# Performance work log

Measured on AMD Instinct MI355X. Metric: run time of the kernel, lower is better.

The kernel has to match this reference:

```python
import jax, jax.numpy as jnp
import numpy as np

D_MODEL = 1024
NUM_HEADS = 16
D_K = D_MODEL // NUM_HEADS


def setup_inputs() -> dict:
    key = jax.random.key(0)
    ks = jax.random.split(key, 11)
    B, S, D = 2, 2048, D_MODEL
    scale = 1.0 / np.sqrt(D)
    inp = {
        'q': jax.random.normal(ks[0], (B, S, D), jnp.float32),
        'k': jax.random.normal(ks[1], (B, S, D), jnp.float32),
        'v': jax.random.normal(ks[2], (B, S, D), jnp.float32),
        'wq': jax.random.normal(ks[3], (D, D), jnp.float32) * scale,
        'bq': jnp.zeros((D,), jnp.float32),
        'wk': jax.random.normal(ks[4], (D, D), jnp.float32) * scale,
        'bk': jnp.zeros((D,), jnp.float32),
        'wv': jax.random.normal(ks[5], (D, D), jnp.float32) * scale,
        'bv': jnp.zeros((D,), jnp.float32),
        'wo': jax.random.normal(ks[6], (D, D), jnp.float32) * scale,
        'bo': jnp.zeros((D,), jnp.float32),
    }
    return inp


def _split_heads(x):
    B, S, _ = x.shape
    return x.reshape(B, S, NUM_HEADS, D_K).transpose(0, 2, 1, 3)  # [B,H,S,dk]


def reference(q, k, v, wq, bq, wk, bk, wv, bv, wo, bo):
    # Linear projections (torch Linear: x @ W^T + b)
    qh = _split_heads(q @ wq.T + bq)
    kh = _split_heads(k @ wk.T + bk)
    vh = _split_heads(v @ wv.T + bv)
    scores = jnp.einsum('bhqd,bhkd->bhqk', qh, kh) / np.sqrt(D_K)
    attn = jax.nn.softmax(scores, axis=-1)  # dropout is identity in eval
    ctx = jnp.einsum('bhqk,bhkd->bhqd', attn, vh)
    B, H, S, dk = ctx.shape
    ctx = ctx.transpose(0, 2, 1, 3).reshape(B, S, H * dk)
    return ctx @ wo.T + bo
```

## Files before the change

### kernel.cpp

```cpp
#include <hip/hip_runtime.h>
#include <hip/hip_bf16.h>
#include <math.h>

#define BATCH 2
#define SEQ   2048
#define DMODEL 1024
#define NHEAD 16
#define DK    64
#define M_TOT (BATCH*SEQ)
#define KDIM  DMODEL

typedef short bf16x8 __attribute__((ext_vector_type(8)));
typedef float f32x4  __attribute__((ext_vector_type(4)));
typedef __hip_bfloat16 bf16;

#define QSCALE 0.18033688011112042f

__device__ inline void gld_lds16(const void* g, void* l) {
    __builtin_amdgcn_global_load_lds(
        (const __attribute__((address_space(1))) unsigned int*)g,
        (__attribute__((address_space(3))) unsigned int*)l, 16, 0, 0);
}

__device__ inline unsigned pack2(float a, float b) {
    union { __hip_bfloat162 h; unsigned u; } t;
    t.h = __float22bfloat162_rn(make_float2(a, b));
    return t.u;
}

__global__ __launch_bounds__(256) void conv_inputs(
    const float* __restrict__ a, const float* __restrict__ b, const float* __restrict__ c,
    bf16* __restrict__ ah, bf16* __restrict__ bh, bf16* __restrict__ ch, int n)
{
    const float* src = blockIdx.y == 0 ? a : (blockIdx.y == 1 ? b : c);
    bf16* dst = blockIdx.y == 0 ? ah : (blockIdx.y == 1 ? bh : ch);
    const int i = (blockIdx.x * 256 + threadIdx.x) * 4;
    if (i < n) {
        float4 v = *(const float4*)(src + i);
        uint2 o;
        o.x = pack2(v.x, v.y);
        o.y = pack2(v.z, v.w);
        *(uint2*)(dst + i) = o;
    }
}

__global__ __launch_bounds__(256) void conv_weights(
    const float* __restrict__ wq, const float* __restrict__ wk,
    const float* __restrict__ wv, const float* __restrict__ wo,
    bf16* __restrict__ wqh, bf16* __restrict__ wkh, bf16* __restrict__ wvh,
    bf16* __restrict__ woh, bf16* __restrict__ wol, int n)
{
    const int t = blockIdx.y;
    const float* src = t == 0 ? wq : (t == 1 ? wk : (t == 2 ? wv : wo));
    bf16* dsth = t == 0 ? wqh : (t == 1 ? wkh : (t == 2 ? wvh : woh));
    const int i = (blockIdx.x * 256 + threadIdx.x) * 4;
    if (i >= n) return;
    float4 v = *(const float4*)(src + i);
    uint2 oh;
    oh.x = pack2(v.x, v.y);
    oh.y = pack2(v.z, v.w);
    *(uint2*)(dsth + i) = oh;
    if (t == 3) {
        float hx = __bfloat162float(__float2bfloat16(v.x));
        float hy = __bfloat162float(__float2bfloat16(v.y));
        float hz = __bfloat162float(__float2bfloat16(v.z));
        float hw = __bfloat162float(__float2bfloat16(v.w));
        uint2 ol;
        ol.x = pack2(v.x - hx, v.y - hy);
        ol.y = pack2(v.z - hz, v.w - hw);
        *(uint2*)(wol + i) = ol;
    }
}

template<int NSPLIT>
__device__ __forceinline__ void gemm_body(
    const bf16* __restrict__ Ah, const bf16* __restrict__ Al,
    const bf16* __restrict__ Wh, const bf16* __restrict__ Wl,
    const float* __restrict__ bias, void* __restrict__ out,
    int layout, float scale, bf16* sA, bf16* sB)
{
    const int tid  = threadIdx.x;
    const int wave = tid >> 6, lane = tid & 63;
    const int ln   = lane & 15, quad = lane >> 4;
    const int wm   = wave >> 1, wn = wave & 1;
    const int row0 = blockIdx.y * 128, col0 = blockIdx.x * 128;

    const int srow = lane >> 2;
    const int clog = (lane & 3) ^ (srow & 3);
    const size_t gA0 = (size_t)(row0 + wave * 16 + srow) * KDIM + clog * 8;
    const size_t gB0 = (size_t)(col0 + wave * 16 + srow) * KDIM + clog * 8;
    const int ldsoff = (wave * 16 + srow) * 64 + (lane & 3) * 16;

    const int swz = (quad ^ (ln & 3)) * 8;

    f32x4 acc[4][4] = {};

    for (int k0 = 0; k0 < KDIM; k0 += 32) {
        __syncthreads();
#pragma unroll
        for (int j = 0; j < 2; ++j) {
            const size_t go = (size_t)k0 + (size_t)j * 64 * KDIM;
            gld_lds16(Ah + gA0 + go, (char*)sA + j * 4096 + ldsoff);
            gld_lds16(Wh + gB0 + go, (char*)sB + j * 4096 + ldsoff);
            if (NSPLIT > 1) {
                gld_lds16(Al + gA0 + go, (char*)sA + 8192 + j * 4096 + ldsoff);
                gld_lds16(Wl + gB0 + go, (char*)sB + 8192 + j * 4096 + ldsoff);
            }
        }
        __syncthreads();

        bf16x8 af[4], bfr[4];
#pragma unroll
        for (int t = 0; t < 4; ++t) {
            af[t]  = *(const bf16x8*)&sA[(wm * 64 + t * 16 + ln) * 32 + swz];
            bfr[t] = *(const bf16x8*)&sB[(wn * 64 + t * 16 + ln) * 32 + swz];
        }
#pragma unroll
        for (int mt = 0; mt < 4; ++mt)
#pragma unroll
            for (int nt = 0; nt < 4; ++nt)
                acc[mt][nt] = __builtin_amdgcn_mfma_f32_16x16x32_bf16(af[mt], bfr[nt], acc[mt][nt], 0, 0, 0);

        if (NSPLIT > 1) {
            bf16x8 cf[4];
#pragma unroll
            for (int t = 0; t < 4; ++t)
                cf[t] = *(const bf16x8*)&sB[4096 + (wn * 64 + t * 16 + ln) * 32 + swz];
#pragma unroll
            for (int mt = 0; mt < 4; ++mt)
#pragma unroll
                for (int nt = 0; nt < 4; ++nt)
                    acc[mt][nt] = __builtin_amdgcn_mfma_f32_16x16x32_bf16(af[mt], cf[nt], acc[mt][nt], 0, 0, 0);
#pragma unroll
            for (int t = 0; t < 4; ++t)
                cf[t] = *(const bf16x8*)&sA[4096 + (wm * 64 + t * 16 + ln) * 32 + swz];
#pragma unroll
            for (int mt = 0; mt < 4; ++mt)
#pragma unroll
                for (int nt = 0; nt < 4; ++nt)
                    acc[mt][nt] = __builtin_amdgcn_mfma_f32_16x16x32_bf16(cf[mt], bfr[nt], acc[mt][nt], 0, 0, 0);
        }
    }

#pragma unroll
    for (int nt = 0; nt < 4; ++nt) {
        const int n = col0 + wn * 64 + nt * 16 + ln;
        const float bv = bias[n];
#pragma unroll
        for (int mt = 0; mt < 4; ++mt) {
#pragma unroll
            for (int r = 0; r < 4; ++r) {
                const int m = row0 + wm * 64 + mt * 16 + quad * 4 + r;
                const float v = (acc[mt][nt][r] + bv) * scale;
                if (layout == 0) {
                    ((float*)out)[(size_t)m * DMODEL + n] = v;
                } else {
                    const int b = m >> 11, s = m & (SEQ - 1);
                    const int h = n >> 6,  d = n & (DK - 1);
                    const int bh = b * NHEAD + h;
                    bf16 hv = __float2bfloat16(v);
                    if (layout == 1)
                        ((bf16*)out)[((size_t)bh * SEQ + s) * DK + d] = hv;
                    else
                        ((bf16*)out)[((size_t)bh * DK + d) * SEQ + s] = hv;
                }
            }
        }
    }
}

struct QKVArgs {
    const bf16* A[3];
    const bf16* W[3];
    const float* bias[3];
    bf16* out[3];
    float scale[3];
    int layout[3];
};

__global__ __launch_bounds__(256) void qkv_gemm(QKVArgs a) {
    __shared__ __align__(16) bf16 sA[128 * 32];
    __shared__ __align__(16) bf16 sB[128 * 32];
    const int z = blockIdx.z;
    gemm_body<1>(a.A[z], nullptr, a.W[z], nullptr, a.bias[z],
                 (void*)a.out[z], a.layout[z], a.scale[z], sA, sB);
}

__global__ __launch_bounds__(256) void gemm_o(
    const bf16* __restrict__ Ah, const bf16* __restrict__ Al,
    const bf16* __restrict__ Wh, const bf16* __restrict__ Wl,
    const float* __restrict__ bias, float* __restrict__ out)
{
    __shared__ __align__(16) bf16 sA[2 * 128 * 32];
    __shared__ __align__(16) bf16 sB[2 * 128 * 32];
    gemm_body<3>(Ah, Al, Wh, Wl, bias, (void*)out, 0, 1.0f, sA, sB);
}

#define LDP 72
#define NKT (SEQ / 64)
__global__ __launch_bounds__(256) void flash_attn_mfma(
    const bf16* __restrict__ Q, const bf16* __restrict__ K,
    const bf16* __restrict__ Vt,
    bf16* __restrict__ ctxh, bf16* __restrict__ ctxl)
{
    __shared__ __align__(16) bf16 Vts[64 * 64];
    __shared__ __align__(16) bf16 Ps[4][32 * LDP];

    const int tid  = threadIdx.x;
    const int wave = tid >> 6, lane = tid & 63;
    const int ln   = lane & 15, quad = lane >> 4;
    const int swl  = ln & 7;
    const int qt   = blockIdx.x;
    const int bh   = blockIdx.y;
    const int b    = bh >> 4, h = bh & (NHEAD - 1);

    const int q0 = qt * 128 + wave * 32;
    const bf16* Qb = Q + ((size_t)bh * SEQ + q0) * DK;
    bf16x8 qf[2][2];
#pragma unroll
    for (int c = 0; c < 2; ++c)
#pragma unroll
        for (int nt = 0; nt < 2; ++nt)
            qf[c][nt] = *(const bf16x8*)(Qb + (size_t)(nt * 16 + ln) * DK + c * 32 + quad * 8);

    f32x4 of[2][4] = {};
    float lp[2] = {0.f, 0.f};

    const int sr  = tid >> 2;
    const int scb = (tid & 3) * 2;
    const int ssw = sr & 7;
    const bf16* Vg0 = Vt + ((size_t)bh * DK + sr) * SEQ;
    const bf16* Kg0 = K + (size_t)bh * SEQ * DK;

    bf16x8 kf[2][4];
#pragma unroll
    for (int c = 0; c < 2; ++c)
#pragma unroll
        for (int mt = 0; mt < 4; ++mt)
            kf[c][mt] = *(const bf16x8*)(Kg0 + (size_t)(mt * 16 + ln) * DK + c * 32 + quad * 8);
    uint4 vp0 = *(const uint4*)(Vg0 + scb * 8);
    uint4 vp1 = *(const uint4*)(Vg0 + scb * 8 + 8);

    for (int kt = 0; kt < NKT; ++kt) {
        __syncthreads();
        *(uint4*)(&Vts[sr * 64 + ((scb    ) ^ ssw) * 8]) = vp0;
        *(uint4*)(&Vts[sr * 64 + ((scb + 1) ^ ssw) * 8]) = vp1;
        __syncthreads();

        const int ktn = (kt + 1) & (NKT - 1);
        bf16x8 kn[2][4];
#pragma unroll
        for (int c = 0; c < 2; ++c)
#pragma unroll
            for (int mt = 0; mt < 4; ++mt)
                kn[c][mt] = *(const bf16x8*)(Kg0 + (size_t)(ktn * 64 + mt * 16 + ln) * DK + c * 32 + quad * 8);
        uint4 vn0 = *(const uint4*)(Vg0 + ktn * 64 + scb * 8);
        uint4 vn1 = *(const uint4*)(Vg0 + ktn * 64 + scb * 8 + 8);

        f32x4 st[4][2] = {};
#pragma unroll
        for (int c = 0; c < 2; ++c)
#pragma unroll
            for (int mt = 0; mt < 4; ++mt)
#pragma unroll
                for (int nt = 0; nt < 2; ++nt)
                    st[mt][nt] = __builtin_amdgcn_mfma_f32_16x16x32_bf16(kf[c][mt], qf[c][nt], st[mt][nt], 0, 0, 0);

#pragma unroll
        for (int mt = 0; mt < 4; ++mt)
#pragma unroll
            for (int nt = 0; nt < 2; ++nt) {
                float p0 = __builtin_amdgcn_exp2f(st[mt][nt][0]);
                float p1 = __builtin_amdgcn_exp2f(st[mt][nt][1]);
                float p2 = __builtin_amdgcn_exp2f(st[mt][nt][2]);
                float p3 = __builtin_amdgcn_exp2f(st[mt][nt][3]);
                lp[nt] += (p0 + p1) + (p2 + p3);
                uint2 uu;
                uu.x = pack2(p0, p1);
                uu.y = pack2(p2, p3);
                *(uint2*)(&Ps[wave][(nt * 16 + ln) * LDP + mt * 16 + quad * 4]) = uu;
            }

#pragma unroll
        for (int c2 = 0; c2 < 2; ++c2) {
            bf16x8 pf0 = *(const bf16x8*)(&Ps[wave][(0 * 16 + ln) * LDP + c2 * 32 + quad * 8]);
            bf16x8 pf1 = *(const bf16x8*)(&Ps[wave][(1 * 16 + ln) * LDP + c2 * 32 + quad * 8]);
#pragma unroll
            for (int nt = 0; nt < 4; ++nt) {
                bf16x8 vf = *(const bf16x8*)(&Vts[(nt * 16 + ln) * 64 + ((c2 * 4 + quad) ^ swl) * 8]);
                of[0][nt] = __builtin_amdgcn_mfma_f32_16x16x32_bf16(pf0, vf, of[0][nt], 0, 0, 0);
                of[1][nt] = __builtin_amdgcn_mfma_f32_16x16x32_bf16(pf1, vf, of[1][nt], 0, 0, 0);
            }
        }

#pragma unroll
        for (int c = 0; c < 2; ++c)
#pragma unroll
            for (int mt = 0; mt < 4; ++mt)
                kf[c][mt] = kn[c][mt];
        vp0 = vn0; vp1 = vn1;
    }

#pragma unroll
    for (int nt = 0; nt < 2; ++nt) {
        lp[nt] += __shfl_xor(lp[nt], 16, 64);
        lp[nt] += __shfl_xor(lp[nt], 32, 64);
    }
    float linv[2][4];
#pragma unroll
    for (int mtP = 0; mtP < 2; ++mtP)
#pragma unroll
        for (int r = 0; r < 4; ++r)
            linv[mtP][r] = 1.0f / __shfl(lp[mtP], quad * 4 + r, 64);

    const size_t base = ((size_t)b * SEQ + q0) * DMODEL + h * DK;
#pragma unroll
    for (int mtP = 0; mtP < 2; ++mtP)
#pragma unroll
        for (int nt = 0; nt < 4; ++nt)
#pragma unroll
            for (int r = 0; r < 4; ++r) {
                const float v = of[mtP][nt][r] * linv[mtP][r];
                const size_t idx = base + (size_t)(mtP * 16 + quad * 4 + r) * DMODEL + nt * 16 + ln;
                bf16 hv = __float2bfloat16(v);
                ctxh[idx] = hv;
                ctxl[idx] = __float2bfloat16(v - __bfloat162float(hv));
            }
}

extern "C" void kernel_launch(void* const* d_in, const int* in_sizes, int n_in,
                              void* d_out, int out_size, void* d_ws, size_t ws_size,
                              hipStream_t stream) {
    const float* q  = (const float*)d_in[0];
    const float* k  = (const float*)d_in[1];
    const float* v  = (const float*)d_in[2];
    const float* wq = (const float*)d_in[3];
    const float* bq = (const float*)d_in[4];
    const float* wk = (const float*)d_in[5];
    const float* bk = (const float*)d_in[6];
    const float* wv = (const float*)d_in[7];
    const float* bv = (const float*)d_in[8];
    const float* wo = (const float*)d_in[9];
    const float* bo = (const float*)d_in[10];
    float* out = (float*)d_out;

    char* ws = (char*)d_ws;
    const size_t MB = 1u << 20;
    bf16* q_hi  = (bf16*)(ws + 0 * MB);
    bf16* k_hi  = (bf16*)(ws + 8 * MB);
    bf16* v_hi  = (bf16*)(ws + 16 * MB);
    bf16* wq_hi = (bf16*)(ws + 24 * MB);
    bf16* wk_hi = (bf16*)(ws + 26 * MB);
    bf16* wv_hi = (bf16*)(ws + 28 * MB);
    bf16* wo_hi = (bf16*)(ws + 30 * MB);
    bf16* wo_lo = (bf16*)(ws + 32 * MB);
    bf16* Qp    = (bf16*)(ws + 34 * MB);
    bf16* Kp    = (bf16*)(ws + 42 * MB);
    bf16* Vpt   = (bf16*)(ws + 50 * MB);
    bf16* ctx_h = (bf16*)(ws + 0 * MB);
    bf16* ctx_l = (bf16*)(ws + 8 * MB);

    const int NX = M_TOT * DMODEL;
    const int NW = DMODEL * DMODEL;

    conv_inputs<<<dim3(NX / 1024, 3), 256, 0, stream>>>(q, k, v, q_hi, k_hi, v_hi, NX);
    conv_weights<<<dim3(NW / 1024, 4), 256, 0, stream>>>(wq, wk, wv, wo,
                                                          wq_hi, wk_hi, wv_hi, wo_hi, wo_lo, NW);

    QKVArgs qa;
    qa.A[0] = q_hi;  qa.A[1] = k_hi;  qa.A[2] = v_hi;
    qa.W[0] = wq_hi; qa.W[1] = wk_hi; qa.W[2] = wv_hi;
    qa.bias[0] = bq; qa.bias[1] = bk; qa.bias[2] = bv;
    qa.out[0] = Qp;  qa.out[1] = Kp;  qa.out[2] = Vpt;
    qa.scale[0] = QSCALE; qa.scale[1] = 1.0f; qa.scale[2] = 1.0f;
    qa.layout[0] = 1; qa.layout[1] = 1; qa.layout[2] = 2;

    dim3 qgrid(DMODEL / 128, M_TOT / 128, 3);
    qkv_gemm<<<qgrid, 256, 0, stream>>>(qa);

    dim3 fgrid(SEQ / 128, BATCH * NHEAD);
    flash_attn_mfma<<<fgrid, 256, 0, stream>>>(Qp, Kp, Vpt, ctx_h, ctx_l);

    dim3 ogrid(DMODEL / 128, M_TOT / 128);
    gemm_o<<<ogrid, 256, 0, stream>>>(ctx_h, ctx_l, wo_hi, wo_lo, bo, out);
}
```

Baseline: 278.2 us.

## Keep softmax probabilities in registers and feed PV via 16x16x16 MFMA

Removes the per-wave LDS staging buffer for the probability tile. The exp2 results are packed into bf16x4 fragments that directly serve as the A operand of 16x16x16 bf16 MFMAs. V fragments are read from LDS with a matching swizzled address. The K-tile loop is also unrolled by two with ping-pong register buffers, which removes the copy of the prefetched K/V registers. The cost is twice as many smaller MFMA instructions for the PV product.

```diff
diff --git a/kernel.cpp b/kernel.cpp
--- a/kernel.cpp
+++ b/kernel.cpp
@@ -11,6 +11,7 @@
 #define KDIM  DMODEL
 
 typedef short bf16x8 __attribute__((ext_vector_type(8)));
+typedef short bf16x4 __attribute__((ext_vector_type(4)));
 typedef float f32x4  __attribute__((ext_vector_type(4)));
 typedef __hip_bfloat16 bf16;
 
@@ -196,7 +197,6 @@
     gemm_body<3>(Ah, Al, Wh, Wl, bias, (void*)out, 0, 1.0f, sA, sB);
 }
 
-#define LDP 72
 #define NKT (SEQ / 64)
 __global__ __launch_bounds__(256) void flash_attn_mfma(
     const bf16* __restrict__ Q, const bf16* __restrict__ K,
@@ -204,12 +204,10 @@
     bf16* __restrict__ ctxh, bf16* __restrict__ ctxl)
 {
     __shared__ __align__(16) bf16 Vts[64 * 64];
-    __shared__ __align__(16) bf16 Ps[4][32 * LDP];
 
     const int tid  = threadIdx.x;
     const int wave = tid >> 6, lane = tid & 63;
     const int ln   = lane & 15, quad = lane >> 4;
-    const int swl  = ln & 7;
     const int qt   = blockIdx.x;
     const int bh   = blockIdx.y;
     const int b    = bh >> 4, h = bh & (NHEAD - 1);
@@ -232,30 +230,36 @@
     const bf16* Vg0 = Vt + ((size_t)bh * DK + sr) * SEQ;
     const bf16* Kg0 = K + (size_t)bh * SEQ * DK;
 
-    bf16x8 kf[2][4];
+    int vaddr[4];
+#pragma unroll
+    for (int mt = 0; mt < 4; ++mt)
+        vaddr[mt] = ln * 64 + (((2 * mt + (quad >> 1)) ^ (ln & 7)) * 8) + (quad & 1) * 4;
+
+    bf16x8 kfA[2][4], kfB[2][4];
+    uint4 vA0, vA1, vB0, vB1;
 #pragma unroll
     for (int c = 0; c < 2; ++c)
 #pragma unroll
         for (int mt = 0; mt < 4; ++mt)
-            kf[c][mt] = *(const bf16x8*)(Kg0 + (size_t)(mt * 16 + ln) * DK + c * 32 + quad * 8);
-    uint4 vp0 = *(const uint4*)(Vg0 + scb * 8);
-    uint4 vp1 = *(const uint4*)(Vg0 + scb * 8 + 8);
-
-    for (int kt = 0; kt < NKT; ++kt) {
+            kfA[c][mt] = *(const bf16x8*)(Kg0 + (size_t)(mt * 16 + ln) * DK + c * 32 + quad * 8);
+    vA0 = *(const uint4*)(Vg0 + scb * 8);
+    vA1 = *(const uint4*)(Vg0 + scb * 8 + 8);
+
+    auto halfiter = [&](int ktc, bf16x8 (&kfc)[2][4], uint4& v0c, uint4& v1c,
+                        bf16x8 (&kfn)[2][4], uint4& v0n, uint4& v1n) {
         __syncthreads();
-        *(uint4*)(&Vts[sr * 64 + ((scb    ) ^ ssw) * 8]) = vp0;
-        *(uint4*)(&Vts[sr * 64 + ((scb + 1) ^ ssw) * 8]) = vp1;
+        *(uint4*)(&Vts[sr * 64 + ((scb    ) ^ ssw) * 8]) = v0c;
+        *(uint4*)(&Vts[sr * 64 + ((scb + 1) ^ ssw) * 8]) = v1c;
         __syncthreads();
 
-        const int ktn = (kt + 1) & (NKT - 1);
-        bf16x8 kn[2][4];
+        const int ktn = (ktc + 1) & (NKT - 1);
 #pragma unroll
         for (int c = 0; c < 2; ++c)
 #pragma unroll
             for (int mt = 0; mt < 4; ++mt)
-                kn[c][mt] = *(const bf16x8*)(Kg0 + (size_t)(ktn * 64 + mt * 16 + ln) * DK + c * 32 + quad * 8);
-        uint4 vn0 = *(const uint4*)(Vg0 + ktn * 64 + scb * 8);
-        uint4 vn1 = *(const uint4*)(Vg0 + ktn * 64 + scb * 8 + 8);
+                kfn[c][mt] = *(const bf16x8*)(Kg0 + (size_t)(ktn * 64 + mt * 16 + ln) * DK + c * 32 + quad * 8);
+        v0n = *(const uint4*)(Vg0 + ktn * 64 + scb * 8);
+        v1n = *(const uint4*)(Vg0 + ktn * 64 + scb * 8 + 8);
 
         f32x4 st[4][2] = {};
 #pragma unroll
@@ -264,8 +268,9 @@
             for (int mt = 0; mt < 4; ++mt)
 #pragma unroll
                 for (int nt = 0; nt < 2; ++nt)
-                    st[mt][nt] = __builtin_amdgcn_mfma_f32_16x16x32_bf16(kf[c][mt], qf[c][nt], st[mt][nt], 0, 0, 0);
-
+                    st[mt][nt] = __builtin_amdgcn_mfma_f32_16x16x32_bf16(kfc[c][mt], qf[c][nt], st[mt][nt], 0, 0, 0);
+
+        bf16x4 aP[4][2];
 #pragma unroll
         for (int mt = 0; mt < 4; ++mt)
 #pragma unroll
@@ -275,30 +280,25 @@
                 float p2 = __builtin_amdgcn_exp2f(st[mt][nt][2]);
                 float p3 = __builtin_amdgcn_exp2f(st[mt][nt][3]);
                 lp[nt] += (p0 + p1) + (p2 + p3);
-                uint2 uu;
-                uu.x = pack2(p0, p1);
-                uu.y = pack2(p2, p3);
-                *(uint2*)(&Ps[wave][(nt * 16 + ln) * LDP + mt * 16 + quad * 4]) = uu;
-            }
-
-#pragma unroll
-        for (int c2 = 0; c2 < 2; ++c2) {
-            bf16x8 pf0 = *(const bf16x8*)(&Ps[wave][(0 * 16 + ln) * LDP + c2 * 32 + quad * 8]);
-            bf16x8 pf1 = *(const bf16x8*)(&Ps[wave][(1 * 16 + ln) * LDP + c2 * 32 + quad * 8]);
-#pragma unroll
-            for (int nt = 0; nt < 4; ++nt) {
-                bf16x8 vf = *(const bf16x8*)(&Vts[(nt * 16 + ln) * 64 + ((c2 * 4 + quad) ^ swl) * 8]);
-                of[0][nt] = __builtin_amdgcn_mfma_f32_16x16x32_bf16(pf0, vf, of[0][nt], 0, 0, 0);
-                of[1][nt] = __builtin_amdgcn_mfma_f32_16x16x32_bf16(pf1, vf, of[1][nt], 0, 0, 0);
-            }
-        }
-
-#pragma unroll
-        for (int c = 0; c < 2; ++c)
-#pragma unroll
-            for (int mt = 0; mt < 4; ++mt)
-                kf[c][mt] = kn[c][mt];
-        vp0 = vn0; vp1 = vn1;
+                union { bf16x4 v; uint2 u; } uu;
+                uu.u.x = pack2(p0, p1);
+                uu.u.y = pack2(p2, p3);
+                aP[mt][nt] = uu.v;
+            }
+
+#pragma unroll
+        for (int mt = 0; mt < 4; ++mt)
+#pragma unroll
+            for (int ntd = 0; ntd < 4; ++ntd) {
+                bf16x4 vf = *(const bf16x4*)(&Vts[vaddr[mt] + ntd * 1024]);
+                of[0][ntd] = __builtin_amdgcn_mfma_f32_16x16x16bf16_1k(aP[mt][0], vf, of[0][ntd], 0, 0, 0);
+                of[1][ntd] = __builtin_amdgcn_mfma_f32_16x16x16bf16_1k(aP[mt][1], vf, of[1][ntd], 0, 0, 0);
+            }
+    };
+
+    for (int kt = 0; kt < NKT; kt += 2) {
+        halfiter(kt,     kfA, vA0, vA1, kfB, vB0, vB1);
+        halfiter(kt + 1, kfB, vB0, vB1, kfA, vA0, vA1);
     }
 
 #pragma unroll
```

Result: no change. 276.7 us (-0.5%).
